# Kernel tuning notes

Hardware: AMD Instinct MI355X
Metric: run time of the kernel (lower is better)

The kernel has to match this reference:

```python
import jax, jax.numpy as jnp
import numpy as np

S, V = 64, 32          # input scalar / vector multiplicities (64x0e + 32x1o)
MID_S, MID_V = 96, 96  # irreps_mid = 64x0e+32x0e + 64x1o+32x1o
NB = 10                # number_of_basis (radial edge scalars)
N_NODES, N_EDGES = 50000, 400000


def _fctp_attr(xs, xv, attr, Ws, Wv):
    # FullyConnectedTensorProduct(x, node_attr='1x0e'): per-irrep-block linear
    # mixing scaled by the scalar attr, path weight 1/sqrt(fan_in).
    os = (xs @ Ws) * attr * (1.0 / np.sqrt(xs.shape[1]))
    ov = jnp.einsum('nui,uk->nki', xv, Wv) * attr[..., None] * (1.0 / np.sqrt(xv.shape[1]))
    return os, ov


def _conv(ns, nv, attr, src, dst, sh, esc,
          Wsc_s, Wsc_v, Wl1_s, Wl1_v, Wfc1, Wfc2, Wl2_s, Wl2_v, Wa):
    # GraphConvolutionWithNodeAttrs: gather -> weighted e3nn TP -> scatter-mean
    N, E = ns.shape[0], src.shape[0]
    # radial MLP (e3nn FullyConnectedNet, silu) -> per-edge tp weights (192)
    h = jax.nn.silu(esc @ Wfc1 * (1.0 / np.sqrt(esc.shape[1])))
    w = h @ Wfc2 * (1.0 / np.sqrt(h.shape[1]))
    w1, w2, w3, w4 = w[:, :64], w[:, 64:128], w[:, 128:160], w[:, 160:192]
    sc_s, sc_v = _fctp_attr(ns, nv, attr, Wsc_s, Wsc_v)   # self connection
    hs, hv = _fctp_attr(ns, nv, attr, Wl1_s, Wl1_v)       # lin1
    gs, gv = hs[src], hv[src]                              # gather by edge_src
    sh0, shv = sh[:, 0:1], sh[:, 1:4]                      # 1x0e, 1x1o edge sh
    # 'uvu' instructions: (0e x 0e -> 0e), (1o x 1o -> 0e), (0e x 1o -> 1o), (1o x 0e -> 1o)
    m_s = jnp.concatenate([
        gs * sh0 * w1,                                                     # [E,64]
        jnp.einsum('evi,ei->ev', gv, shv) * (1.0 / np.sqrt(3.0)) * w4],   # [E,32]
        axis=1)                                                            # [E,96]
    m_v = jnp.concatenate([
        gs[:, :, None] * shv[:, None, :] * w2[:, :, None],  # [E,64,3]
        gv * sh0[:, :, None] * w3[:, :, None]],              # [E,32,3]
        axis=1)                                              # [E,96,3]
    # scatter with reduce='mean' onto destination nodes
    deg = jnp.maximum(jax.ops.segment_sum(jnp.ones((E,), ns.dtype), dst, num_segments=N), 1.0)
    Ms = jax.ops.segment_sum(m_s, dst, num_segments=N) / deg[:, None]
    Mv = jax.ops.segment_sum(m_v, dst, num_segments=N) / deg[:, None, None]
    alpha = (Ms @ Wa) * (1.0 / np.sqrt(MID_S)) * attr      # [N,1] (output_mask==1)
    os, ov = _fctp_attr(Ms, Mv, attr, Wl2_s, Wl2_v)        # lin2
    return sc_s + alpha * os, sc_v + alpha[..., None] * ov


def _forward(node_s, node_v, node_attr, edge_src, edge_dst, edge_sh, edge_scalars, p1, p2):
    s, v = _conv(node_s, node_v, node_attr, edge_src, edge_dst, edge_sh, edge_scalars, *p1)
    # Gate: 64 scalars (silu) | 32 gates (sigmoid) gating 32x1o vectors
    gs = jax.nn.silu(s[:, :64])
    v = v * jax.nn.sigmoid(s[:, 64:96])[:, :, None]
    s2, v2 = _conv(gs, v, node_attr, edge_src, edge_dst, edge_sh, edge_scalars, *p2)
    return jnp.concatenate([s2, v2.reshape(v2.shape[0], -1)], axis=1)  # [N,160]


def setup_inputs():
    ks = jax.random.split(jax.random.key(0), 32)
    N, E = N_NODES, N_EDGES
    g = lambda i, shape: jax.random.normal(ks[i], shape, jnp.float32)
    inp = {'node_s': g(0, (N, S)),
           'node_v': g(1, (N, V, 3)),
           'node_attr': jnp.ones((N, 1), jnp.float32),
           'edge_src': jax.random.randint(ks[2], (E,), 0, N),
           'edge_dst': jax.random.randint(ks[3], (E,), 0, N),
           'edge_sh': g(4, (E, 4)),
           'edge_scalars': jax.random.uniform(ks[5], (E, NB), jnp.float32)}
    dims = {1: (96, 32), 2: (64, 32)}  # layer1 conv out feeds gate; layer2 is final conv
    i = 6
    for L in (1, 2):
        o_s, o_v = dims[L]
        for name, shape in [('sc_s', (S, o_s)), ('sc_v', (V, o_v)), ('lin1_s', (S, S)),
                            ('lin1_v', (V, V)), ('fc1', (NB, 64)), ('fc2', (64, 192)),
                            ('lin2_s', (MID_S, o_s)), ('lin2_v', (MID_V, o_v)), ('alpha', (MID_S, 1))]:
            inp['l%d_%s' % (L, name)] = g(i, shape)
            i += 1
    return inp


def reference(node_s, node_v, node_attr, edge_src, edge_dst, edge_sh, edge_scalars,
              l1_sc_s, l1_sc_v, l1_lin1_s, l1_lin1_v, l1_fc1, l1_fc2, l1_lin2_s, l1_lin2_v, l1_alpha,
              l2_sc_s, l2_sc_v, l2_lin1_s, l2_lin1_v, l2_fc1, l2_fc2, l2_lin2_s, l2_lin2_v, l2_alpha):
    p1 = (l1_sc_s, l1_sc_v, l1_lin1_s, l1_lin1_v, l1_fc1, l1_fc2, l1_lin2_s, l1_lin2_v, l1_alpha)
    p2 = (l2_sc_s, l2_sc_v, l2_lin1_s, l2_lin1_v, l2_fc1, l2_fc2, l2_lin2_s, l2_lin2_v, l2_alpha)
    return _forward(node_s, node_v, node_attr, edge_src, edge_dst, edge_sh, edge_scalars, p1, p2)
```

## Files before the change

kernel.cpp:

```cpp
#include <hip/hip_runtime.h>
#include <hip/hip_bf16.h>

#define INV_SQRT10 0.31622776601683794f
#define INV_SQRT64 0.125f
#define INV_SQRT32 0.17677669529663687f
#define INV_SQRT96 0.10206207261596575f
#define INV_SQRT3  0.5773502691896258f

typedef __attribute__((ext_vector_type(4))) float f32x4;
typedef __attribute__((ext_vector_type(8))) short bf16x8;

__device__ __forceinline__ unsigned short f2bf(float x) {
    return __builtin_bit_cast(unsigned short, (__hip_bfloat16)x);
}
__device__ __forceinline__ float bf2f(unsigned short u) {
    union { unsigned u; float f; } v; v.u = ((unsigned)u) << 16;
    return v.f;
}

__global__ __launch_bounds__(256) void k_prep_nodes(
    const float* __restrict__ ns, const float* __restrict__ nv,
    const int* __restrict__ dst,
    unsigned short* __restrict__ xsb, unsigned short* __restrict__ xvpb,
    int* __restrict__ cnt, int N, int E)
{
    const int gid = blockIdx.x * 256 + threadIdx.x, gs = gridDim.x * 256;
    for (int i = gid; i < N * 64; i += gs) xsb[i] = f2bf(ns[i]);
    for (int i = gid; i < N * 96; i += gs) {
        const int n = i / 96, rem = i - n * 96;
        const int ic = rem >> 5, u = rem & 31;
        xvpb[i] = f2bf(nv[(size_t)n * 96 + u * 3 + ic]);
    }
    for (int i = gid; i < E; i += gs) atomicAdd(&cnt[dst[i]], 1);
}

template <int OS>
__global__ __launch_bounds__(256) void k_prep_w(
    const float* __restrict__ Wl1s, const float* __restrict__ Wscs,
    const float* __restrict__ Wl1v, const float* __restrict__ Wscv,
    const float* __restrict__ Wfc2,
    const float* __restrict__ W2s, const float* __restrict__ W2v,
    const float* __restrict__ Wa,
    unsigned short* __restrict__ wsb, unsigned short* __restrict__ wvb,
    unsigned short* __restrict__ wfb,
    unsigned short* __restrict__ wob, unsigned short* __restrict__ wv2b)
{
    constexpr int NC1 = 64 + OS;
    constexpr int PC1 = ((OS + 16 + 15) / 16) * 16;
    const int gid = blockIdx.x * 256 + threadIdx.x, gs = gridDim.x * 256;
    for (int i = gid; i < NC1 * 64; i += gs) {
        const int c = i >> 6, k = i & 63;
        const float v = (c < 64) ? Wl1s[k * 64 + c] : Wscs[k * OS + (c - 64)];
        wsb[i] = f2bf(v);
    }
    for (int i = gid; i < 64 * 32; i += gs) {
        const int c = i >> 5, u = i & 31;
        const float v = (c < 32) ? Wl1v[u * 32 + c] : Wscv[u * 32 + (c - 32)];
        wvb[i] = f2bf(v);
    }
    for (int i = gid; i < 192 * 64; i += gs) {
        const int c = i >> 6, k = i & 63;
        wfb[i] = f2bf(Wfc2[k * 192 + c]);
    }
    for (int i = gid; i < PC1 * 96; i += gs) {
        const int c = i / 96, u = i - c * 96;
        float v = 0.f;
        if (c < OS) v = W2s[u * OS + c];
        else if (c == OS) v = Wa[u];
        wob[i] = f2bf(v);
    }
    for (int i = gid; i < 32 * 96; i += gs) {
        const int c = i / 96, u = i - c * 96;
        wv2b[i] = f2bf(W2v[u * 32 + c]);
    }
}

__global__ __launch_bounds__(256) void k_scan1(const int* __restrict__ cnt,
                                               int* __restrict__ partial, int N)
{
    __shared__ int lds[256];
    const int t = threadIdx.x, i = blockIdx.x * 256 + t;
    int v = (i < N) ? cnt[i] : 0;
    lds[t] = v;
    __syncthreads();
    for (int off = 128; off > 0; off >>= 1) {
        if (t < off) lds[t] += lds[t + off];
        __syncthreads();
    }
    if (t == 0) partial[blockIdx.x] = lds[0];
}

__global__ __launch_bounds__(1024) void k_scan2(int* __restrict__ partial, int NB)
{
    __shared__ int lds[1024];
    const int t = threadIdx.x;
    int v = (t < NB) ? partial[t] : 0;
    lds[t] = v;
    __syncthreads();
    for (int off = 1; off < 1024; off <<= 1) {
        int w = (t >= off) ? lds[t - off] : 0;
        __syncthreads();
        lds[t] += w;
        __syncthreads();
    }
    if (t < NB) partial[t] = lds[t] - v;
}

__global__ __launch_bounds__(256) void k_scan3(const int* __restrict__ cnt,
                                               const int* __restrict__ partial,
                                               int* __restrict__ base, int N)
{
    __shared__ int lds[256];
    const int t = threadIdx.x, i = blockIdx.x * 256 + t;
    int v = (i < N) ? cnt[i] : 0;
    lds[t] = v;
    __syncthreads();
    for (int off = 1; off < 256; off <<= 1) {
        int w = (t >= off) ? lds[t - off] : 0;
        __syncthreads();
        lds[t] += w;
        __syncthreads();
    }
    if (i < N) base[i] = partial[blockIdx.x] + lds[t] - v;
}

__global__ __launch_bounds__(256) void k_order(
    const int* __restrict__ dst, const int* __restrict__ base,
    int* __restrict__ cursor, int* __restrict__ order, int E)
{
    int i = blockIdx.x * 256 + threadIdx.x;
    if (i < E) {
        const int d = dst[i];
        order[base[d] + atomicAdd(&cursor[d], 1)] = i;
    }
}

__global__ __launch_bounds__(256) void k_gather(
    const int* __restrict__ order,
    const int* __restrict__ src, const float* __restrict__ sh,
    const float* __restrict__ esc,
    int* __restrict__ src_ord, float4* __restrict__ sh_ord,
    unsigned short* __restrict__ esc_ordb, int E)
{
    int pos = blockIdx.x * 256 + threadIdx.x;
    if (pos < E) {
        const int e = order[pos];
        src_ord[pos] = src[e];
        sh_ord[pos] = ((const float4*)sh)[e];
        const float* ep = esc + (size_t)e * 10;
        unsigned short* eo = esc_ordb + (size_t)pos * 10;
        #pragma unroll
        for (int q = 0; q < 10; q++) eo[q] = f2bf(ep[q]);
    }
}

template <int OS>
__global__ __launch_bounds__(256) void k_node_mfma(
    const unsigned short* __restrict__ xsb, const unsigned short* __restrict__ xvpb,
    const float* __restrict__ attr,
    const unsigned short* __restrict__ wsb, const unsigned short* __restrict__ wvb,
    unsigned short* __restrict__ hsb, unsigned short* __restrict__ hvbb4,
    unsigned short* __restrict__ scs, unsigned short* __restrict__ scv, int N)
{
    constexpr int NC1 = 64 + OS;
    constexpr int CT1 = NC1 / 16;
    __shared__ float attr_l[64];
    const int tid = threadIdx.x;
    const int n0 = blockIdx.x * 64;
    if (tid < 64) attr_l[tid] = (n0 + tid < N) ? attr[n0 + tid] : 0.f;
    __syncthreads();
    const int wv = tid >> 6, lane = tid & 63;
    const int mrow = lane & 15, kg = lane >> 4;

    {
        const int rbase = wv * 16;
        const int r = rbase + mrow;
        const int rc = min(n0 + r, N - 1);
        const bf16x8 a0 = *(const bf16x8*)(xsb + (size_t)rc * 64 + kg * 8);
        const bf16x8 a1 = *(const bf16x8*)(xsb + (size_t)rc * 64 + 32 + kg * 8);
        f32x4 acc[CT1];
        #pragma unroll
        for (int t = 0; t < CT1; t++) acc[t] = (f32x4){0.f, 0.f, 0.f, 0.f};
        #pragma unroll
        for (int t = 0; t < CT1; t++) {
            const int c = t * 16 + mrow;
            const bf16x8 b0 = *(const bf16x8*)(wsb + c * 64 + kg * 8);
            const bf16x8 b1 = *(const bf16x8*)(wsb + c * 64 + 32 + kg * 8);
            acc[t] = __builtin_amdgcn_mfma_f32_16x16x32_bf16(a0, b0, acc[t], 0, 0, 0);
            acc[t] = __builtin_amdgcn_mfma_f32_16x16x32_bf16(a1, b1, acc[t], 0, 0, 0);
        }
        #pragma unroll
        for (int t = 0; t < CT1; t++) {
            const int c = t * 16 + mrow;
            #pragma unroll
            for (int rg = 0; rg < 4; rg++) {
                const int row = rbase + kg * 4 + rg;
                const int n = n0 + row;
                if (n < N) {
                    const float v = acc[t][rg] * INV_SQRT64 * attr_l[row];
                    if (c < 64) hsb[(size_t)n * 64 + c] = f2bf(v);
                    else        scs[(size_t)n * OS + (c - 64)] = f2bf(v);
                }
            }
        }
    }
    #pragma unroll
    for (int j = 0; j < 3; j++) {
        const int rbase = (wv * 3 + j) * 16;
        const int rv = rbase + mrow;
        const int ic = rv >> 6, nloc = rv & 63;
        const int nc = min(n0 + nloc, N - 1);
        const bf16x8 a = *(const bf16x8*)(xvpb + (size_t)nc * 96 + ic * 32 + kg * 8);
        f32x4 acc2[4];
        #pragma unroll
        for (int t = 0; t < 4; t++) acc2[t] = (f32x4){0.f, 0.f, 0.f, 0.f};
        #pragma unroll
        for (int t = 0; t < 4; t++) {
            const int c = t * 16 + mrow;
            const bf16x8 b = *(const bf16x8*)(wvb + c * 32 + kg * 8);
            acc2[t] = __builtin_amdgcn_mfma_f32_16x16x32_bf16(a, b, acc2[t], 0, 0, 0);
        }
        #pragma unroll
        for (int t = 0; t < 4; t++) {
            const int c = t * 16 + mrow;
            #pragma unroll
            for (int rg = 0; rg < 4; rg++) {
                const int rv2 = rbase + kg * 4 + rg;
                const int ic2 = rv2 >> 6, nl = rv2 & 63;
                const int n = n0 + nl;
                if (n < N) {
                    const float v = acc2[t][rg] * INV_SQRT32 * attr_l[nl];
                    if (c < 32) hvbb4[(size_t)n * 128 + c * 4 + ic2] = f2bf(v);
                    else        scv[(size_t)n * 96 + ic2 * 32 + (c - 32)] = f2bf(v);
                }
            }
        }
    }
}

__global__ __launch_bounds__(256) void k_edge_mlp(
    const unsigned short* __restrict__ esc_ordb, const int* __restrict__ base,
    const float* __restrict__ Wfc1, const unsigned short* __restrict__ wfb,
    unsigned* __restrict__ wbuf12, unsigned short* __restrict__ wbufB,
    int n0, int n1, int N, int E, int cap)
{
    __shared__ float w1_l[640];
    __shared__ __align__(16) char hb[64 * 64 * 2];
    __shared__ __align__(16) char wf_l[192 * 64 * 2];
    const int tid = threadIdx.x;
    const int lo = (n0 == 0) ? 0 : base[n0];
    const int hi = (n1 >= N) ? E : base[n1];
    const int p0 = lo + blockIdx.x * 64;
    if (p0 >= hi) return;

    for (int i = tid; i < 640; i += 256) w1_l[i] = Wfc1[i];
    for (int i = tid; i < 1536; i += 256) {
        const int c = i >> 3, k16 = i & 7;
        const uint4 v = *(const uint4*)(wfb + c * 64 + k16 * 8);
        *(uint4*)(wf_l + (((c << 7) + (k16 << 4)) ^ ((c & 7) << 4))) = v;
    }
    const int r = tid >> 2, c0 = (tid & 3) << 4;
    float ev[10];
    {
        const int rc = min(p0 + r, E - 1);
        const unsigned* ep = (const unsigned*)(esc_ordb + (size_t)rc * 10);
        #pragma unroll
        for (int q = 0; q < 5; q++) {
            const unsigned u = ep[q];
            ev[2 * q]     = bf2f((unsigned short)(u & 0xFFFF));
            ev[2 * q + 1] = bf2f((unsigned short)(u >> 16));
        }
    }
    __syncthreads();
    {
        float hval[16];
        #pragma unroll
        for (int c = 0; c < 16; c++) {
            float acc = 0.f;
            #pragma unroll
            for (int q = 0; q < 10; q++) acc += ev[q] * w1_l[q * 64 + c0 + c];
            acc *= INV_SQRT10;
            hval[c] = acc / (1.f + __expf(-acc));
        }
        unsigned pk[8];
        #pragma unroll
        for (int j = 0; j < 8; j++)
            pk[j] = (unsigned)f2bf(hval[2 * j]) | ((unsigned)f2bf(hval[2 * j + 1]) << 16);
        const int swz = (r & 7) << 4;
        const int b0 = (r << 7) + (c0 << 1);
        *(uint4*)(hb + (b0 ^ swz)) = make_uint4(pk[0], pk[1], pk[2], pk[3]);
        *(uint4*)(hb + ((b0 + 16) ^ swz)) = make_uint4(pk[4], pk[5], pk[6], pk[7]);
    }
    __syncthreads();
    const int wv = tid >> 6, lane = tid & 63;
    const int mrow = lane & 15, kgrp = lane >> 4;
    f32x4 acc[12];
    #pragma unroll
    for (int t = 0; t < 12; t++) acc[t] = (f32x4){0.f, 0.f, 0.f, 0.f};
    #pragma unroll
    for (int kc = 0; kc < 2; kc++) {
        const int rr = wv * 16 + mrow;
        const int abyte = ((rr << 7) + (kc << 6) + (kgrp << 4)) ^ ((rr & 7) << 4);
        const bf16x8 afrag = *(const bf16x8*)(hb + abyte);
        #pragma unroll
        for (int t = 0; t < 12; t++) {
            const int c = t * 16 + mrow;
            const int bbyte = ((c << 7) + (kc << 6) + (kgrp << 4)) ^ ((c & 7) << 4);
            const bf16x8 bfrag = *(const bf16x8*)(wf_l + bbyte);
            acc[t] = __builtin_amdgcn_mfma_f32_16x16x32_bf16(afrag, bfrag, acc[t], 0, 0, 0);
        }
    }
    #pragma unroll
    for (int rg = 0; rg < 4; rg++) {
        const int rloc = wv * 16 + kgrp * 4 + rg;
        const int pos = p0 + rloc;
        if (pos < hi && (pos - lo) < cap) {
            uint4 pk12;
            pk12.x = (unsigned)f2bf(acc[0][rg] * INV_SQRT64) | ((unsigned)f2bf(acc[4][rg] * INV_SQRT64) << 16);
            pk12.y = (unsigned)f2bf(acc[1][rg] * INV_SQRT64) | ((unsigned)f2bf(acc[5][rg] * INV_SQRT64) << 16);
            pk12.z = (unsigned)f2bf(acc[2][rg] * INV_SQRT64) | ((unsigned)f2bf(acc[6][rg] * INV_SQRT64) << 16);
            pk12.w = (unsigned)f2bf(acc[3][rg] * INV_SQRT64) | ((unsigned)f2bf(acc[7][rg] * INV_SQRT64) << 16);
            ushort4 pkB;
            pkB.x = f2bf(acc[8][rg] * INV_SQRT64);
            pkB.y = f2bf(acc[9][rg] * INV_SQRT64);
            pkB.z = f2bf(acc[10][rg] * INV_SQRT64);
            pkB.w = f2bf(acc[11][rg] * INV_SQRT64);
            *(uint4*)(wbuf12 + (size_t)(pos - lo) * 64 + mrow * 4) = pk12;
            *(ushort4*)(wbufB + (size_t)(pos - lo) * 64 + mrow * 4) = pkB;
        }
    }
}

__global__ __launch_bounds__(256) void k_agg(
    const unsigned short* __restrict__ hsb, const unsigned short* __restrict__ hvbb4,
    const int* __restrict__ src_ord, const float4* __restrict__ sh_ord,
    const int* __restrict__ base, const int* __restrict__ cnt,
    const unsigned* __restrict__ wbuf12, const unsigned short* __restrict__ wbufB,
    unsigned short* __restrict__ Msb, unsigned short* __restrict__ Mvb,
    int n0, int n1, int N, int E)
{
    const int wave = threadIdx.x >> 6, lane = threadIdx.x & 63;
    const int n = n0 + blockIdx.x * 4 + wave;
    if (n >= n1) return;
    const int lo = (n0 == 0) ? 0 : base[n0];
    const int cidx = (lane & 15) * 4 + (lane >> 4);

    float aS = 0.f, aSB = 0.f;
    float aV0 = 0.f, aV1 = 0.f, aV2 = 0.f;
    float aB0 = 0.f, aB1 = 0.f, aB2 = 0.f;
    const int b0 = base[n];
    const int c_ = cnt[n];
    const size_t wb = (size_t)(b0 - lo) * 64;

    for (int j0 = 0; j0 < c_; j0 += 4) {
        const int m = c_ - j0;
        int sidx[4];
        unsigned p12[4];
        float wB[4], gs[4];
        ushort4 gv[4];
        float4 s4[4];
        #pragma unroll
        for (int k = 0; k < 4; k++)
            if (k < m) sidx[k] = src_ord[b0 + j0 + k];
        #pragma unroll
        for (int k = 0; k < 4; k++) {
            if (k < m) {
                p12[k] = wbuf12[wb + (size_t)(j0 + k) * 64 + cidx];
                wB[k] = bf2f(wbufB[wb + (size_t)(j0 + k) * 64 + cidx]);
                gs[k] = bf2f(hsb[(size_t)sidx[k] * 64 + lane]);
                if (lane < 32)
                    gv[k] = *(const ushort4*)(hvbb4 + (size_t)sidx[k] * 128 + lane * 4);
                else
                    gv[k] = make_ushort4(0, 0, 0, 0);
                s4[k] = sh_ord[b0 + j0 + k];
            }
        }
        #pragma unroll
        for (int k = 0; k < 4; k++) {
            if (k < m) {
                const float w1 = bf2f((unsigned short)(p12[k] & 0xFFFF));
                const float w2 = bf2f((unsigned short)(p12[k] >> 16));
                const float g0 = bf2f(gv[k].x), g1 = bf2f(gv[k].y), g2 = bf2f(gv[k].z);
                const float gvdot = g0 * s4[k].y + g1 * s4[k].z + g2 * s4[k].w;
                const float gvd = __shfl(gvdot, lane & 31);
                aS  += gs[k] * s4[k].x * w1;
                aSB += gvd * INV_SQRT3 * wB[k];
                aV0 += gs[k] * s4[k].y * w2;
                aV1 += gs[k] * s4[k].z * w2;
                aV2 += gs[k] * s4[k].w * w2;
                aB0 += g0 * s4[k].x * wB[k];
                aB1 += g1 * s4[k].x * wB[k];
                aB2 += g2 * s4[k].x * wB[k];
            }
        }
    }
    const float invd = 1.f / (float)max(c_, 1);
    unsigned short* msp = Msb + (size_t)n * 96;
    unsigned short* mvp = Mvb + (size_t)n * 3 * 96;
    msp[lane] = f2bf(aS * invd);
    if (lane >= 32) msp[64 + (lane - 32)] = f2bf(aSB * invd);
    mvp[0 * 96 + lane] = f2bf(aV0 * invd);
    mvp[1 * 96 + lane] = f2bf(aV1 * invd);
    mvp[2 * 96 + lane] = f2bf(aV2 * invd);
    if (lane < 32) {
        mvp[0 * 96 + 64 + lane] = f2bf(aB0 * invd);
        mvp[1 * 96 + 64 + lane] = f2bf(aB1 * invd);
        mvp[2 * 96 + 64 + lane] = f2bf(aB2 * invd);
    }
}

template <int OS, bool FINAL>
__global__ __launch_bounds__(256) void k_node_out(
    const unsigned short* __restrict__ Msb, const unsigned short* __restrict__ Mvb,
    const float* __restrict__ attr,
    const unsigned short* __restrict__ scs, const unsigned short* __restrict__ scv,
    const unsigned short* __restrict__ wob, const unsigned short* __restrict__ wv2b,
    float* __restrict__ outF,
    unsigned short* __restrict__ outSb, unsigned short* __restrict__ outVb, int N)
{
    constexpr int CT1 = (OS + 16 + 15) / 16;
    constexpr int TA = OS / 16;
    __shared__ float attr_l[64];
    __shared__ float alpha_l[64];
    __shared__ float gate_l[64][32];
    const int tid = threadIdx.x;
    const int n0 = blockIdx.x * 64;
    if (tid < 64) attr_l[tid] = (n0 + tid < N) ? attr[n0 + tid] : 0.f;
    __syncthreads();
    const int wv = tid >> 6, lane = tid & 63;
    const int mrow = lane & 15, kg = lane >> 4;

    const int rbase = wv * 16;
    const int rc = min(n0 + rbase + mrow, N - 1);
    f32x4 acc[CT1];
    #pragma unroll
    for (int t = 0; t < CT1; t++) acc[t] = (f32x4){0.f, 0.f, 0.f, 0.f};
    #pragma unroll
    for (int kc = 0; kc < 3; kc++) {
        const bf16x8 a = *(const bf16x8*)(Msb + (size_t)rc * 96 + kc * 32 + kg * 8);
        #pragma unroll
        for (int t = 0; t < CT1; t++) {
            const bf16x8 b = *(const bf16x8*)(wob + (size_t)(t * 16 + mrow) * 96 + kc * 32 + kg * 8);
            acc[t] = __builtin_amdgcn_mfma_f32_16x16x32_bf16(a, b, acc[t], 0, 0, 0);
        }
    }
    if (mrow == 0) {
        #pragma unroll
        for (int rg = 0; rg < 4; rg++) {
            const int row = rbase + kg * 4 + rg;
            alpha_l[row] = acc[TA][rg] * INV_SQRT96 * attr_l[row];
        }
    }
    __syncthreads();
    #pragma unroll
    for (int t = 0; t < CT1; t++) {
        const int c = t * 16 + mrow;
        if (c < OS) {
            #pragma unroll
            for (int rg = 0; rg < 4; rg++) {
                const int row = rbase + kg * 4 + rg;
                const int n = n0 + row;
                if (n < N) {
                    const float os = acc[t][rg] * INV_SQRT96 * attr_l[row];
                    const float s = bf2f(scs[(size_t)n * OS + c]) + alpha_l[row] * os;
                    if (FINAL) {
                        outF[(size_t)n * 160 + c] = s;
                    } else {
                        if (c < 64) outSb[(size_t)n * 64 + c] = f2bf(s / (1.f + __expf(-s)));
                        else        gate_l[row][c - 64] = 1.f / (1.f + __expf(-s));
                    }
                }
            }
        }
    }
    __syncthreads();
    #pragma unroll
    for (int j = 0; j < 3; j++) {
        const int rb2 = (wv * 3 + j) * 16;
        const int rv = rb2 + mrow;
        const int nl = rv / 3, ii = rv - nl * 3;
        const int nc2 = min(n0 + nl, N - 1);
        f32x4 acc2[2];
        acc2[0] = (f32x4){0.f, 0.f, 0.f, 0.f};
        acc2[1] = (f32x4){0.f, 0.f, 0.f, 0.f};
        #pragma unroll
        for (int kc = 0; kc < 3; kc++) {
            const bf16x8 a = *(const bf16x8*)(Mvb + ((size_t)nc2 * 3 + ii) * 96 + kc * 32 + kg * 8);
            #pragma unroll
            for (int t = 0; t < 2; t++) {
                const bf16x8 b = *(const bf16x8*)(wv2b + (size_t)(t * 16 + mrow) * 96 + kc * 32 + kg * 8);
                acc2[t] = __builtin_amdgcn_mfma_f32_16x16x32_bf16(a, b, acc2[t], 0, 0, 0);
            }
        }
        #pragma unroll
        for (int t = 0; t < 2; t++) {
            const int k = t * 16 + mrow;
            #pragma unroll
            for (int rg = 0; rg < 4; rg++) {
                const int rv2 = rb2 + kg * 4 + rg;
                const int nl2 = rv2 / 3, i2 = rv2 - nl2 * 3;
                const int n = n0 + nl2;
                if (n < N) {
                    const float ov = acc2[t][rg] * INV_SQRT96 * attr_l[nl2];
                    const float v = bf2f(scv[(size_t)n * 96 + i2 * 32 + k]) + alpha_l[nl2] * ov;
                    if (FINAL) outF[(size_t)n * 160 + 64 + k * 3 + i2] = v;
                    else       outVb[(size_t)n * 96 + i2 * 32 + k] = f2bf(v * gate_l[nl2][k]);
                }
            }
        }
    }
}

extern "C" void kernel_launch(void* const* d_in, const int* in_sizes, int n_in,
                              void* d_out, int out_size, void* d_ws, size_t ws_size,
                              hipStream_t stream)
{
    const float* node_s = (const float*)d_in[0];
    const float* node_v = (const float*)d_in[1];
    const float* attr   = (const float*)d_in[2];
    const int*   esrc   = (const int*)d_in[3];
    const int*   edst   = (const int*)d_in[4];
    const float* esh    = (const float*)d_in[5];
    const float* esc    = (const float*)d_in[6];
    const float* W[18];
    for (int i = 0; i < 18; i++) W[i] = (const float*)d_in[7 + i];

    const int N = in_sizes[0] / 64;
    const int E = in_sizes[3];
    const int NB = (N + 255) / 256;

    char* p = (char*)d_ws;
    unsigned short* xsb  = (unsigned short*)p; p += (size_t)N * 64 * 2;
    unsigned short* xvpb = (unsigned short*)p; p += (size_t)N * 96 * 2;
    unsigned short* hsb  = (unsigned short*)p; p += (size_t)N * 64 * 2;
    unsigned short* hvbb4 = (unsigned short*)p; p += (size_t)N * 128 * 2;
    unsigned short* Msb  = (unsigned short*)p; p += (size_t)N * 96 * 2;
    unsigned short* Mvb  = (unsigned short*)p; p += (size_t)N * 288 * 2;
    unsigned short* scs  = (unsigned short*)p; p += (size_t)N * 96 * 2;
    unsigned short* scv  = (unsigned short*)p; p += (size_t)N * 96 * 2;
    unsigned short* wsb1 = (unsigned short*)p; p += 160 * 64 * 2;
    unsigned short* wsb2 = (unsigned short*)p; p += 128 * 64 * 2;
    unsigned short* wvb1 = (unsigned short*)p; p += 64 * 32 * 2;
    unsigned short* wvb2 = (unsigned short*)p; p += 64 * 32 * 2;
    unsigned short* wfb1 = (unsigned short*)p; p += 192 * 64 * 2;
    unsigned short* wfb2 = (unsigned short*)p; p += 192 * 64 * 2;
    unsigned short* wob1 = (unsigned short*)p; p += 112 * 96 * 2;
    unsigned short* wob2 = (unsigned short*)p; p += 80 * 96 * 2;
    unsigned short* wv2b1 = (unsigned short*)p; p += 32 * 96 * 2;
    unsigned short* wv2b2 = (unsigned short*)p; p += 32 * 96 * 2;
    int* cnt    = (int*)p; p += (size_t)N * 4;
    int* cursor = (int*)p; p += (size_t)N * 4;
    int* basei  = (int*)p; p += (size_t)N * 4;
    int* partial = (int*)p; p += (size_t)NB * 4;
    p = (char*)(((size_t)p + 255) & ~(size_t)255);
    int* order   = (int*)p; p += (size_t)E * 4;
    int* src_ord = (int*)p; p += (size_t)E * 4;
    p = (char*)(((size_t)p + 15) & ~(size_t)15);
    float4* sh_ord = (float4*)p; p += (size_t)E * 16;
    unsigned short* esc_ordb = (unsigned short*)p; p += (size_t)E * 20;
    p = (char*)(((size_t)p + 255) & ~(size_t)255);
    const size_t used_fixed = (size_t)(p - (char*)d_ws);

    int NQ = 4;
    size_t cap = 0;
    {
        const int cands[3] = {1, 2, 4};
        for (int ci = 0; ci < 3; ci++) {
            const int c = cands[ci];
            size_t cc = (c == 1) ? (size_t)E : ((size_t)E / c) * 9 / 8 + 256;
            if (used_fixed + cc * 384 <= ws_size) { NQ = c; cap = cc; break; }
        }
        if (cap == 0) { NQ = 4; cap = ((size_t)E / 4) * 9 / 8 + 256; }
    }
    unsigned* wbuf12      = (unsigned*)p;       p += cap * 256;
    unsigned short* wbufB = (unsigned short*)p; p += cap * 128;

    const int nb  = (N + 63) / 64;
    const int ebk = (E + 255) / 256;
    const int Q   = (N + NQ - 1) / NQ;
    const int qb  = (Q + 3) / 4;
    const int emb = (int)((cap + 63) / 64);

    hipMemsetAsync(cnt, 0, (size_t)2 * N * sizeof(int), stream);
    k_prep_nodes<<<2048, 256, 0, stream>>>(node_s, node_v, edst, xsb, xvpb, cnt, N, E);
    k_prep_w<96><<<32, 256, 0, stream>>>(W[2], W[0], W[3], W[1], W[5], W[6], W[7], W[8],
                                         wsb1, wvb1, wfb1, wob1, wv2b1);
    k_prep_w<64><<<32, 256, 0, stream>>>(W[11], W[9], W[12], W[10], W[14], W[15], W[16], W[17],
                                         wsb2, wvb2, wfb2, wob2, wv2b2);
    k_scan1<<<NB, 256, 0, stream>>>(cnt, partial, N);
    k_scan2<<<1, 1024, 0, stream>>>(partial, NB);
    k_scan3<<<NB, 256, 0, stream>>>(cnt, partial, basei, N);
    k_order<<<ebk, 256, 0, stream>>>(edst, basei, cursor, order, E);
    k_gather<<<ebk, 256, 0, stream>>>(order, esrc, esh, esc,
                                      src_ord, sh_ord, esc_ordb, E);

    k_node_mfma<96><<<nb, 256, 0, stream>>>(xsb, xvpb, attr, wsb1, wvb1,
                                            hsb, hvbb4, scs, scv, N);
    for (int q = 0; q < NQ; q++) {
        const int n0 = q * Q, n1 = min(N, (q + 1) * Q);
        if (n0 >= n1) break;
        k_edge_mlp<<<emb, 256, 0, stream>>>(esc_ordb, basei, W[4], wfb1,
                                            wbuf12, wbufB, n0, n1, N, E, (int)cap);
        k_agg<<<qb, 256, 0, stream>>>(hsb, hvbb4, src_ord, sh_ord, basei, cnt,
                                      wbuf12, wbufB, Msb, Mvb, n0, n1, N, E);
    }
    k_node_out<96, false><<<nb, 256, 0, stream>>>(Msb, Mvb, attr, scs, scv,
                                                  wob1, wv2b1,
                                                  nullptr, xsb, xvpb, N);
    k_node_mfma<64><<<nb, 256, 0, stream>>>(xsb, xvpb, attr, wsb2, wvb2,
                                            hsb, hvbb4, scs, scv, N);
    for (int q = 0; q < NQ; q++) {
        const int n0 = q * Q, n1 = min(N, (q + 1) * Q);
        if (n0 >= n1) break;
        k_edge_mlp<<<emb, 256, 0, stream>>>(esc_ordb, basei, W[13], wfb2,
                                            wbuf12, wbufB, n0, n1, N, E, (int)cap);
        k_agg<<<qb, 256, 0, stream>>>(hsb, hvbb4, src_ord, sh_ord, basei, cnt,
                                      wbuf12, wbufB, Msb, Mvb, n0, n1, N, E);
    }
    k_node_out<64, true><<<nb, 256, 0, stream>>>(Msb, Mvb, attr, scs, scv,
                                                 wob2, wv2b2,
                                                 (float*)d_out, nullptr, nullptr, N);
}
```

Measured before the change: 484.1 us.

## Process two destination nodes per wave in k_agg with software-prefetched edge loads

Each wavefront in the aggregation kernel now handles two destination nodes instead of one. It interleaves their edge loops and prefetches the next edge's weights, gathered features, sh and the source index two edges ahead. The goal is more independent memory requests in flight per wave, to hide gather latency, where the old code used a 4-wide unrolled batch per node. The cost is more registers, and wasted iterations when the two nodes' degrees differ. The grid size is halved to match.

```diff
diff --git a/kernel.cpp b/kernel.cpp
--- a/kernel.cpp
+++ b/kernel.cpp
@@ -340,72 +340,136 @@
     int n0, int n1, int N, int E)
 {
     const int wave = threadIdx.x >> 6, lane = threadIdx.x & 63;
-    const int n = n0 + blockIdx.x * 4 + wave;
-    if (n >= n1) return;
+    const int nA = n0 + blockIdx.x * 8 + wave * 2;
+    const int nB = nA + 1;
+    const bool vA = nA < n1, vB = nB < n1;
+    if (!vA) return;
     const int lo = (n0 == 0) ? 0 : base[n0];
     const int cidx = (lane & 15) * 4 + (lane >> 4);
 
-    float aS = 0.f, aSB = 0.f;
-    float aV0 = 0.f, aV1 = 0.f, aV2 = 0.f;
-    float aB0 = 0.f, aB1 = 0.f, aB2 = 0.f;
-    const int b0 = base[n];
-    const int c_ = cnt[n];
-    const size_t wb = (size_t)(b0 - lo) * 64;
-
-    for (int j0 = 0; j0 < c_; j0 += 4) {
-        const int m = c_ - j0;
-        int sidx[4];
-        unsigned p12[4];
-        float wB[4], gs[4];
-        ushort4 gv[4];
-        float4 s4[4];
-        #pragma unroll
-        for (int k = 0; k < 4; k++)
-            if (k < m) sidx[k] = src_ord[b0 + j0 + k];
-        #pragma unroll
-        for (int k = 0; k < 4; k++) {
-            if (k < m) {
-                p12[k] = wbuf12[wb + (size_t)(j0 + k) * 64 + cidx];
-                wB[k] = bf2f(wbufB[wb + (size_t)(j0 + k) * 64 + cidx]);
-                gs[k] = bf2f(hsb[(size_t)sidx[k] * 64 + lane]);
-                if (lane < 32)
-                    gv[k] = *(const ushort4*)(hvbb4 + (size_t)sidx[k] * 128 + lane * 4);
-                else
-                    gv[k] = make_ushort4(0, 0, 0, 0);
-                s4[k] = sh_ord[b0 + j0 + k];
+    float accA[8] = {0.f, 0.f, 0.f, 0.f, 0.f, 0.f, 0.f, 0.f};
+    float accB[8] = {0.f, 0.f, 0.f, 0.f, 0.f, 0.f, 0.f, 0.f};
+    const int bA = base[nA], cA = cnt[nA];
+    const int bB = vB ? base[nB] : 0, cB = vB ? cnt[nB] : 0;
+    const size_t wbA = (size_t)(bA - lo) * 64;
+    const size_t wbB = (size_t)(bB - lo) * 64;
+    const int cmax = max(cA, cB);
+
+    unsigned pA = 0; float wA = 0.f, gsA = 0.f;
+    float ga0 = 0.f, ga1 = 0.f, ga2 = 0.f;
+    float4 sa = make_float4(0.f, 0.f, 0.f, 0.f);
+    int sA2 = 0;
+    if (cA > 0) {
+        const int s1 = src_ord[bA];
+        sA2 = (cA > 1) ? src_ord[bA + 1] : 0;
+        pA = wbuf12[wbA + cidx];
+        wA = bf2f(wbufB[wbA + cidx]);
+        gsA = bf2f(hsb[(size_t)s1 * 64 + lane]);
+        if (lane < 32) {
+            const ushort4 g = *(const ushort4*)(hvbb4 + (size_t)s1 * 128 + lane * 4);
+            ga0 = bf2f(g.x); ga1 = bf2f(g.y); ga2 = bf2f(g.z);
+        }
+        sa = sh_ord[bA];
+    }
+    unsigned pB = 0; float wB = 0.f, gsB = 0.f;
+    float gb0 = 0.f, gb1 = 0.f, gb2 = 0.f;
+    float4 sb = make_float4(0.f, 0.f, 0.f, 0.f);
+    int sB2 = 0;
+    if (cB > 0) {
+        const int s1 = src_ord[bB];
+        sB2 = (cB > 1) ? src_ord[bB + 1] : 0;
+        pB = wbuf12[wbB + cidx];
+        wB = bf2f(wbufB[wbB + cidx]);
+        gsB = bf2f(hsb[(size_t)s1 * 64 + lane]);
+        if (lane < 32) {
+            const ushort4 g = *(const ushort4*)(hvbb4 + (size_t)s1 * 128 + lane * 4);
+            gb0 = bf2f(g.x); gb1 = bf2f(g.y); gb2 = bf2f(g.z);
+        }
+        sb = sh_ord[bB];
+    }
+
+    for (int j = 0; j < cmax; ++j) {
+        unsigned pAn = 0; float wAn = 0.f, gsAn = 0.f;
+        float ga0n = 0.f, ga1n = 0.f, ga2n = 0.f;
+        float4 san = make_float4(0.f, 0.f, 0.f, 0.f);
+        if (j + 1 < cA) {
+            pAn = wbuf12[wbA + (size_t)(j + 1) * 64 + cidx];
+            wAn = bf2f(wbufB[wbA + (size_t)(j + 1) * 64 + cidx]);
+            gsAn = bf2f(hsb[(size_t)sA2 * 64 + lane]);
+            if (lane < 32) {
+                const ushort4 g = *(const ushort4*)(hvbb4 + (size_t)sA2 * 128 + lane * 4);
+                ga0n = bf2f(g.x); ga1n = bf2f(g.y); ga2n = bf2f(g.z);
             }
-        }
-        #pragma unroll
-        for (int k = 0; k < 4; k++) {
-            if (k < m) {
-                const float w1 = bf2f((unsigned short)(p12[k] & 0xFFFF));
-                const float w2 = bf2f((unsigned short)(p12[k] >> 16));
-                const float g0 = bf2f(gv[k].x), g1 = bf2f(gv[k].y), g2 = bf2f(gv[k].z);
-                const float gvdot = g0 * s4[k].y + g1 * s4[k].z + g2 * s4[k].w;
-                const float gvd = __shfl(gvdot, lane & 31);
-                aS  += gs[k] * s4[k].x * w1;
-                aSB += gvd * INV_SQRT3 * wB[k];
-                aV0 += gs[k] * s4[k].y * w2;
-                aV1 += gs[k] * s4[k].z * w2;
-                aV2 += gs[k] * s4[k].w * w2;
-                aB0 += g0 * s4[k].x * wB[k];
-                aB1 += g1 * s4[k].x * wB[k];
-                aB2 += g2 * s4[k].x * wB[k];
+            san = sh_ord[bA + j + 1];
+        }
+        const int sA2n = (j + 2 < cA) ? src_ord[bA + j + 2] : 0;
+        unsigned pBn = 0; float wBn = 0.f, gsBn = 0.f;
+        float gb0n = 0.f, gb1n = 0.f, gb2n = 0.f;
+        float4 sbn = make_float4(0.f, 0.f, 0.f, 0.f);
+        if (j + 1 < cB) {
+            pBn = wbuf12[wbB + (size_t)(j + 1) * 64 + cidx];
+            wBn = bf2f(wbufB[wbB + (size_t)(j + 1) * 64 + cidx]);
+            gsBn = bf2f(hsb[(size_t)sB2 * 64 + lane]);
+            if (lane < 32) {
+                const ushort4 g = *(const ushort4*)(hvbb4 + (size_t)sB2 * 128 + lane * 4);
+                gb0n = bf2f(g.x); gb1n = bf2f(g.y); gb2n = bf2f(g.z);
             }
-        }
-    }
-    const float invd = 1.f / (float)max(c_, 1);
-    unsigned short* msp = Msb + (size_t)n * 96;
-    unsigned short* mvp = Mvb + (size_t)n * 3 * 96;
-    msp[lane] = f2bf(aS * invd);
-    if (lane >= 32) msp[64 + (lane - 32)] = f2bf(aSB * invd);
-    mvp[0 * 96 + lane] = f2bf(aV0 * invd);
-    mvp[1 * 96 + lane] = f2bf(aV1 * invd);
-    mvp[2 * 96 + lane] = f2bf(aV2 * invd);
-    if (lane < 32) {
-        mvp[0 * 96 + 64 + lane] = f2bf(aB0 * invd);
-        mvp[1 * 96 + 64 + lane] = f2bf(aB1 * invd);
-        mvp[2 * 96 + 64 + lane] = f2bf(aB2 * invd);
+            sbn = sh_ord[bB + j + 1];
+        }
+        const int sB2n = (j + 2 < cB) ? src_ord[bB + j + 2] : 0;
+        if (j < cA) {
+            const float w1 = bf2f((unsigned short)(pA & 0xFFFF));
+            const float w2 = bf2f((unsigned short)(pA >> 16));
+            const float gvdot = ga0 * sa.y + ga1 * sa.z + ga2 * sa.w;
+            const float gvd = __shfl(gvdot, lane & 31);
+            accA[0] += gsA * sa.x * w1;
+            accA[1] += gvd * INV_SQRT3 * wA;
+            accA[2] += gsA * sa.y * w2;
+            accA[3] += gsA * sa.z * w2;
+            accA[4] += gsA * sa.w * w2;
+            accA[5] += ga0 * sa.x * wA;
+            accA[6] += ga1 * sa.x * wA;
+            accA[7] += ga2 * sa.x * wA;
+        }
+        if (j < cB) {
+            const float w1 = bf2f((unsigned short)(pB & 0xFFFF));
+            const float w2 = bf2f((unsigned short)(pB >> 16));
+            const float gvdot = gb0 * sb.y + gb1 * sb.z + gb2 * sb.w;
+            const float gvd = __shfl(gvdot, lane & 31);
+            accB[0] += gsB * sb.x * w1;
+            accB[1] += gvd * INV_SQRT3 * wB;
+            accB[2] += gsB * sb.y * w2;
+            accB[3] += gsB * sb.z * w2;
+            accB[4] += gsB * sb.w * w2;
+            accB[5] += gb0 * sb.x * wB;
+            accB[6] += gb1 * sb.x * wB;
+            accB[7] += gb2 * sb.x * wB;
+        }
+        pA = pAn; wA = wAn; gsA = gsAn; ga0 = ga0n; ga1 = ga1n; ga2 = ga2n;
+        sa = san; sA2 = sA2n;
+        pB = pBn; wB = wBn; gsB = gsBn; gb0 = gb0n; gb1 = gb1n; gb2 = gb2n;
+        sb = sbn; sB2 = sB2n;
+    }
+    #pragma unroll
+    for (int h = 0; h < 2; h++) {
+        const float* acc = h ? accB : accA;
+        const int n = h ? nB : nA;
+        const int c_ = h ? cB : cA;
+        const bool v_ = h ? vB : vA;
+        if (!v_) continue;
+        const float invd = 1.f / (float)max(c_, 1);
+        unsigned short* msp = Msb + (size_t)n * 96;
+        unsigned short* mvp = Mvb + (size_t)n * 3 * 96;
+        msp[lane] = f2bf(acc[0] * invd);
+        if (lane >= 32) msp[64 + (lane - 32)] = f2bf(acc[1] * invd);
+        mvp[0 * 96 + lane] = f2bf(acc[2] * invd);
+        mvp[1 * 96 + lane] = f2bf(acc[3] * invd);
+        mvp[2 * 96 + lane] = f2bf(acc[4] * invd);
+        if (lane < 32) {
+            mvp[0 * 96 + 64 + lane] = f2bf(acc[5] * invd);
+            mvp[1 * 96 + 64 + lane] = f2bf(acc[6] * invd);
+            mvp[2 * 96 + 64 + lane] = f2bf(acc[7] * invd);
+        }
     }
 }
 
@@ -578,7 +642,7 @@
     const int nb  = (N + 63) / 64;
     const int ebk = (E + 255) / 256;
     const int Q   = (N + NQ - 1) / NQ;
-    const int qb  = (Q + 3) / 4;
+    const int qb  = (Q + 7) / 8;
     const int emb = (int)((cap + 63) / 64);
 
     hipMemsetAsync(cnt, 0, (size_t)2 * N * sizeof(int), stream);
```

After: 495.9 us. 2.4% more time.
